# Kernel tuning notes

Measured on AMD Instinct MI355X. Metric: run time of the kernel, lower is better.

## Reference

```python
import jax, jax.numpy as jnp
import numpy as np

N_NODES = 100000
N_EDGES = 3200000
NUM_FEATURES = 512
HIDDEN = 16
NUM_CLASSES = 32


def _gcn_conv(x, src, dst, norm, W, b, n):
    # PyG GCNConv: linear transform first, then normalized scatter-add aggregation
    xw = x @ W                          # [N, out]
    msg = xw[src] * norm[:, None]       # gather over edges (incl. self-loops)
    agg = jax.ops.segment_sum(msg, dst, num_segments=n)
    return agg + b


def setup_inputs() -> dict:
    key = jax.random.key(0)
    k_x, k_e, k_w1, k_w2 = jax.random.split(key, 4)
    x = jax.random.normal(k_x, (N_NODES, NUM_FEATURES), dtype=jnp.float32)
    edge_index = jax.random.randint(k_e, (2, N_EDGES), 0, N_NODES, dtype=jnp.int64)
    # Glorot-style init for the two GCNConv weights; zero bias (PyG default)
    W1 = jax.random.normal(k_w1, (NUM_FEATURES, HIDDEN), dtype=jnp.float32) * (1.0 / np.sqrt(NUM_FEATURES))
    b1 = jnp.zeros((HIDDEN,), dtype=jnp.float32)
    W2 = jax.random.normal(k_w2, (HIDDEN, NUM_CLASSES), dtype=jnp.float32) * (1.0 / np.sqrt(HIDDEN))
    b2 = jnp.zeros((NUM_CLASSES,), dtype=jnp.float32)
    return {"x": x, "edge_index": edge_index, "W1": W1, "b1": b1, "W2": W2, "b2": b2}


def reference(x, edge_index, W1, b1, W2, b2):
    n = x.shape[0]
    # add self-loops (PyG GCNConv default add_self_loops=True)
    loops = jnp.arange(n, dtype=edge_index.dtype)
    src = jnp.concatenate([edge_index[0], loops])
    dst = jnp.concatenate([edge_index[1], loops])
    # symmetric normalization D^{-1/2} (A+I) D^{-1/2}
    deg = jax.ops.segment_sum(jnp.ones_like(dst, dtype=x.dtype), dst, num_segments=n)
    dinv = jnp.where(deg > 0, jax.lax.rsqrt(deg), 0.0)
    norm = dinv[src] * dinv[dst]        # [E + N]

    h = jax.nn.relu(_gcn_conv(x, src, dst, norm, W1, b1, n))
    # F.dropout(p=0.5, training=self.training): eval mode -> identity
    out = _gcn_conv(h, src, dst, norm, W2, b2, n)
    return (out, h)
```

## Files before the change

kernel.cpp:

```cpp
#include <hip/hip_runtime.h>
#include <hip/hip_fp16.h>


#define NN 100000
#define NE 3200000
#define FIN 512
#define HID 16
#define NCLS 32
#define NB 391
#define NBP 512
#define CAP_B 9216

#define OFF_BCNT  0
#define OFF_START (NBP)
#define OFF_CNT   (NBP + NN)
#define OFF_DINV  (NBP + 2*NN)
#define OFF_EP    (NBP + 3*NN)
#define OFF_XWS   (OFF_EP + NB*CAP_B)
#define OFF_HSC   (OFF_XWS + NN*8)

__global__ __launch_bounds__(512) void k_binA(const int* __restrict__ src,
                                              const int* __restrict__ dst,
                                              int* __restrict__ bcnt,
                                              unsigned* __restrict__ ep) {
    __shared__ int hist[NBP];
    __shared__ int gpos[NBP];
    int tid = threadIdx.x;
    hist[tid] = 0;
    __syncthreads();
    int base = blockIdx.x * 4096;
    unsigned rec[8];
    int meta[8];
#pragma unroll
    for (int k = 0; k < 8; ++k) {
        int e = base + tid + k * 512;
        if (e < NE) {
            int s = __builtin_nontemporal_load(src + e);
            int d = __builtin_nontemporal_load(dst + e);
            int b = d >> 8;
            int p = atomicAdd(&hist[b], 1);
            rec[k] = ((unsigned)s << 8) | (unsigned)(d & 255);
            meta[k] = (p << 9) | b;
        } else meta[k] = -1;
    }
    __syncthreads();
    int v = hist[tid];
    if (v > 0) gpos[tid] = atomicAdd(&bcnt[tid], v);
    __syncthreads();
#pragma unroll
    for (int k = 0; k < 8; ++k) {
        if (meta[k] >= 0) {
            int b = meta[k] & 511;
            int p = meta[k] >> 9;
            ep[b * CAP_B + gpos[b] + p] = rec[k];
        }
    }
}

__global__ __launch_bounds__(256) void k_binB(unsigned* __restrict__ ep,
                                              const int* __restrict__ bcnt,
                                              int* __restrict__ startA,
                                              int* __restrict__ cntA,
                                              float* __restrict__ dinv) {
    __shared__ int nh[256];
    __shared__ int ns[256];
    __shared__ int np_[256];
    __shared__ int esL[CAP_B];
    int tid = threadIdx.x;
    int b = blockIdx.x;
    int gbase = b * CAP_B;
    int bc = bcnt[b];
    if (bc > CAP_B) bc = CAP_B;
    nh[tid] = 0;
    __syncthreads();
    for (int t = tid; t < bc; t += 256)
        atomicAdd(&nh[ep[gbase + t] & 255], 1);
    __syncthreads();
    int v = nh[tid];
    ns[tid] = v;
    __syncthreads();
#pragma unroll
    for (int o = 1; o < 256; o <<= 1) {
        int u = (tid >= o) ? ns[tid - o] : 0;
        __syncthreads();
        ns[tid] += u;
        __syncthreads();
    }
    int ex = ns[tid] - v;
    np_[tid] = ex;
    __syncthreads();
    for (int t = tid; t < bc; t += 256) {
        unsigned r = ep[gbase + t];
        int dl = r & 255;
        int p = atomicAdd(&np_[dl], 1);
        esL[p] = (int)(r >> 8);
    }
    __syncthreads();
    for (int t = tid; t < bc; t += 256)
        ep[gbase + t] = (unsigned)esL[t];
    int node = b * 256 + tid;
    if (node < NN) {
        startA[node] = gbase + ex;
        cntA[node]   = v;
        dinv[node]   = rsqrtf((float)(v + 1));
    }
}

__global__ __launch_bounds__(256) void k_xw(const float* __restrict__ x,
                                            const float* __restrict__ W1,
                                            const float* __restrict__ dinv,
                                            __half* __restrict__ xws) {
    __shared__ float w1[FIN * HID];
    for (int t = threadIdx.x; t < FIN * HID; t += 256) {
        int k = t >> 4, j = t & 15;
        int s = (k * 4 + ((j >> 2) ^ ((k >> 2) & 3))) * 4 + (j & 3);
        w1[s] = W1[t];
    }
    __syncthreads();
    int w  = threadIdx.x >> 6;
    int nl = (threadIdx.x >> 2) & 15;
    int c  = threadIdx.x & 3;
    int n0 = blockIdx.x * 128 + w * 32 + nl;
    int n1 = n0 + 16;
    bool v0 = n0 < NN, v1 = n1 < NN;
    const float4* x4 = reinterpret_cast<const float4*>(x);
    const float4* r0 = x4 + (v0 ? (size_t)n0 * (FIN / 4) : 0);
    const float4* r1 = x4 + (v1 ? (size_t)n1 * (FIN / 4) : 0);
    const float4* wv = reinterpret_cast<const float4*>(w1);
    float a0[HID], a1[HID];
#pragma unroll
    for (int j = 0; j < HID; ++j) { a0[j] = 0.f; a1[j] = 0.f; }
#pragma unroll 4
    for (int t = 0; t < 32; ++t) {
        int qk = c + 4 * t;
        float4 xv0 = r0[qk];
        float4 xv1 = r1[qk];
        const float4* wb = wv + qk * 16;
#pragma unroll
        for (int e = 0; e < 4; ++e) {
            float xe0 = (e == 0) ? xv0.x : (e == 1) ? xv0.y : (e == 2) ? xv0.z : xv0.w;
            float xe1 = (e == 0) ? xv1.x : (e == 1) ? xv1.y : (e == 2) ? xv1.z : xv1.w;
#pragma unroll
            for (int j4 = 0; j4 < 4; ++j4) {
                float4 w4 = wb[e * 4 + (j4 ^ c)];
                a0[j4 * 4 + 0] += xe0 * w4.x;
                a0[j4 * 4 + 1] += xe0 * w4.y;
                a0[j4 * 4 + 2] += xe0 * w4.z;
                a0[j4 * 4 + 3] += xe0 * w4.w;
                a1[j4 * 4 + 0] += xe1 * w4.x;
                a1[j4 * 4 + 1] += xe1 * w4.y;
                a1[j4 * 4 + 2] += xe1 * w4.z;
                a1[j4 * 4 + 3] += xe1 * w4.w;
            }
        }
    }
#pragma unroll
    for (int j = 0; j < HID; ++j) {
        a0[j] += __shfl_xor(a0[j], 1);
        a0[j] += __shfl_xor(a0[j], 2);
        a1[j] += __shfl_xor(a1[j], 1);
        a1[j] += __shfl_xor(a1[j], 2);
    }
    if (c == 0) {
        if (v0) {
            float dv = dinv[n0];
            __half2 hv[8];
#pragma unroll
            for (int k = 0; k < 8; ++k)
                hv[k] = __floats2half2_rn(a0[2 * k] * dv, a0[2 * k + 1] * dv);
            float4* o = reinterpret_cast<float4*>(xws + (size_t)n0 * HID);
            o[0] = *reinterpret_cast<float4*>(&hv[0]);
            o[1] = *reinterpret_cast<float4*>(&hv[4]);
        }
        if (v1) {
            float dv = dinv[n1];
            __half2 hv[8];
#pragma unroll
            for (int k = 0; k < 8; ++k)
                hv[k] = __floats2half2_rn(a1[2 * k] * dv, a1[2 * k + 1] * dv);
            float4* o = reinterpret_cast<float4*>(xws + (size_t)n1 * HID);
            o[0] = *reinterpret_cast<float4*>(&hv[0]);
            o[1] = *reinterpret_cast<float4*>(&hv[4]);
        }
    }
}

__global__ __launch_bounds__(256) void k_gather1(const int* __restrict__ startA,
                                                 const int* __restrict__ cntA,
                                                 const int* __restrict__ esrc,
                                                 const __half2* __restrict__ xws2,
                                                 const float* __restrict__ dinv,
                                                 const float* __restrict__ b1,
                                                 float* __restrict__ hout,
                                                 __half2* __restrict__ hsc2) {
    int wave = (blockIdx.x * 256 + threadIdx.x) >> 6;
    if (wave >= NN) return;
    int i = wave;
    int lane = threadIdx.x & 63;
    int j2 = lane & 7;
    int c = lane >> 3;
    int st = startA[i], en = st + cntA[i];
    float sx[8], sy[8];
#pragma unroll
    for (int k = 0; k < 8; ++k) { sx[k] = 0.f; sy[k] = 0.f; }
    for (int e = st + c; e < en; e += 64) {
        int a[8];
#pragma unroll
        for (int k = 0; k < 8; ++k) {
            int ee = e + 8 * k;
            a[k] = __builtin_nontemporal_load(esrc + (ee < en ? ee : e));
        }
#pragma unroll
        for (int k = 0; k < 8; ++k) {
            float2 f = __half22float2(xws2[a[k] * 8 + j2]);
            bool ok = (e + 8 * k) < en;
            sx[k] += ok ? f.x : 0.f;
            sy[k] += ok ? f.y : 0.f;
        }
    }
    float sumx = ((sx[0] + sx[1]) + (sx[2] + sx[3])) + ((sx[4] + sx[5]) + (sx[6] + sx[7]));
    float sumy = ((sy[0] + sy[1]) + (sy[2] + sy[3])) + ((sy[4] + sy[5]) + (sy[6] + sy[7]));
    sumx += __shfl_xor(sumx, 8);  sumy += __shfl_xor(sumy, 8);
    sumx += __shfl_xor(sumx, 16); sumy += __shfl_xor(sumy, 16);
    sumx += __shfl_xor(sumx, 32); sumy += __shfl_xor(sumy, 32);
    if (c == 0) {
        float dv = dinv[i];
        float2 self = __half22float2(xws2[i * 8 + j2]);
        float vx = b1[2 * j2]     + dv * (sumx + self.x);
        float vy = b1[2 * j2 + 1] + dv * (sumy + self.y);
        float hx = vx > 0.f ? vx : 0.f;
        float hy = vy > 0.f ? vy : 0.f;
        *reinterpret_cast<float2*>(hout + i * HID + 2 * j2) = make_float2(hx, hy);
        hsc2[i * 8 + j2] = __floats2half2_rn(hx * dv, hy * dv);
    }
}

__global__ __launch_bounds__(256) void k_gather2h(const int* __restrict__ startA,
                                                  const int* __restrict__ cntA,
                                                  const int* __restrict__ esrc,
                                                  const __half2* __restrict__ hsc2,
                                                  const float* __restrict__ dinv,
                                                  const float* __restrict__ W2,
                                                  const float* __restrict__ b2,
                                                  float* __restrict__ out) {
    __shared__ float w2s[HID * NCLS];
    __shared__ float b2s[NCLS];
    for (int t = threadIdx.x; t < HID * NCLS; t += 256) w2s[t] = W2[t];
    if (threadIdx.x < NCLS) b2s[threadIdx.x] = b2[threadIdx.x];
    __syncthreads();
    int wave = (blockIdx.x * 256 + threadIdx.x) >> 6;
    if (wave >= NN) return;
    int i = wave;
    int lane = threadIdx.x & 63;
    int j2 = lane & 7;
    int c = lane >> 3;
    int st = startA[i], en = st + cntA[i];
    float sx[8], sy[8];
#pragma unroll
    for (int k = 0; k < 8; ++k) { sx[k] = 0.f; sy[k] = 0.f; }
    for (int e = st + c; e < en; e += 64) {
        int a[8];
#pragma unroll
        for (int k = 0; k < 8; ++k) {
            int ee = e + 8 * k;
            a[k] = __builtin_nontemporal_load(esrc + (ee < en ? ee : e));
        }
#pragma unroll
        for (int k = 0; k < 8; ++k) {
            float2 f = __half22float2(hsc2[a[k] * 8 + j2]);
            bool ok = (e + 8 * k) < en;
            sx[k] += ok ? f.x : 0.f;
            sy[k] += ok ? f.y : 0.f;
        }
    }
    float sumx = ((sx[0] + sx[1]) + (sx[2] + sx[3])) + ((sx[4] + sx[5]) + (sx[6] + sx[7]));
    float sumy = ((sy[0] + sy[1]) + (sy[2] + sy[3])) + ((sy[4] + sy[5]) + (sy[6] + sy[7]));
    sumx += __shfl_xor(sumx, 8);  sumy += __shfl_xor(sumy, 8);
    sumx += __shfl_xor(sumx, 16); sumy += __shfl_xor(sumy, 16);
    sumx += __shfl_xor(sumx, 32); sumy += __shfl_xor(sumy, 32);
    {
        float2 self = __half22float2(hsc2[i * 8 + j2]);
        sumx += self.x;
        sumy += self.y;
    }
    int jo = lane & 31;
    float acc = 0.f;
#pragma unroll
    for (int p = 0; p < 8; ++p) {
        acc += __shfl(sumx, p) * w2s[(2 * p) * NCLS + jo];
        acc += __shfl(sumy, p) * w2s[(2 * p + 1) * NCLS + jo];
    }
    if (lane < 32)
        out[i * NCLS + jo] = b2s[jo] + dinv[i] * acc;
}

extern "C" void kernel_launch(void* const* d_in, const int* in_sizes, int n_in,
                              void* d_out, int out_size, void* d_ws, size_t ws_size,
                              hipStream_t stream) {
    const float* x  = (const float*)d_in[0];
    const int* ei   = (const int*)d_in[1];
    const float* W1 = (const float*)d_in[2];
    const float* b1 = (const float*)d_in[3];
    const float* W2 = (const float*)d_in[4];
    const float* b2 = (const float*)d_in[5];

    const int* src = ei;
    const int* dst = ei + NE;

    int* wsi = (int*)d_ws;
    int*      bcnt  = wsi + OFF_BCNT;
    int*      startA= wsi + OFF_START;
    int*      cntA  = wsi + OFF_CNT;
    float*    dinv  = (float*)(wsi + OFF_DINV);
    unsigned* ep    = (unsigned*)(wsi + OFF_EP);
    __half*   xws   = (__half*)(wsi + OFF_XWS);
    __half2*  xws2  = (__half2*)(wsi + OFF_XWS);
    __half2*  hsc2  = (__half2*)(wsi + OFF_HSC);

    float* outp = (float*)d_out;
    float* hout = outp + NN * NCLS;

    const int B = 256;

    hipMemsetAsync(bcnt, 0, NBP * sizeof(int), stream);
    hipLaunchKernelGGL(k_binA,  dim3((NE + 4095) / 4096), dim3(512), 0, stream, src, dst, bcnt, ep);
    hipLaunchKernelGGL(k_binB,  dim3(NB), dim3(B), 0, stream, ep, bcnt, startA, cntA, dinv);
    hipLaunchKernelGGL(k_xw,    dim3((NN + 127) / 128), dim3(B), 0, stream, x, W1, dinv, xws);
    hipLaunchKernelGGL(k_gather1, dim3((NN * 64 + B - 1) / B), dim3(B), 0, stream,
                       startA, cntA, (const int*)ep, xws2, dinv, b1, hout, hsc2);
    hipLaunchKernelGGL(k_gather2h, dim3((NN * 64 + B - 1) / B), dim3(B), 0, stream,
                       startA, cntA, (const int*)ep, hsc2, dinv, W2, b2, outp);
}
```

Baseline: 202.7 us.

## Stage binned edges in LDS before global scatter; store W1 as half in LDS

The binning kernel now does a block-local prefix sum over bucket counts and sorts records into shared memory by bucket. It then writes them to global memory in bucket-contiguous order, so the scattered global stores become more coalesced. Separately, the x@W1 kernel keeps W1 in shared memory as packed fp16 with an XOR swizzle, which halves LDS footprint and load traffic per FMA. The cost is extra conversion work, a 9-step scan with barriers, and reduced precision on the weights.

```diff
diff --git a/kernel.cpp b/kernel.cpp
--- a/kernel.cpp
+++ b/kernel.cpp
@@ -24,36 +24,57 @@
                                               int* __restrict__ bcnt,
                                               unsigned* __restrict__ ep) {
     __shared__ int hist[NBP];
+    __shared__ int lstart[NBP];
     __shared__ int gpos[NBP];
+    __shared__ unsigned recs[4096];
+    __shared__ unsigned short bkt[4096];
     int tid = threadIdx.x;
     hist[tid] = 0;
     __syncthreads();
     int base = blockIdx.x * 4096;
     unsigned rec[8];
-    int meta[8];
+    int bk[8], pl[8];
 #pragma unroll
     for (int k = 0; k < 8; ++k) {
         int e = base + tid + k * 512;
         if (e < NE) {
             int s = __builtin_nontemporal_load(src + e);
             int d = __builtin_nontemporal_load(dst + e);
-            int b = d >> 8;
-            int p = atomicAdd(&hist[b], 1);
+            bk[k] = d >> 8;
+            pl[k] = atomicAdd(&hist[bk[k]], 1);
             rec[k] = ((unsigned)s << 8) | (unsigned)(d & 255);
-            meta[k] = (p << 9) | b;
-        } else meta[k] = -1;
+        } else bk[k] = -1;
     }
     __syncthreads();
     int v = hist[tid];
+    lstart[tid] = v;
+    __syncthreads();
+#pragma unroll
+    for (int o = 1; o < 512; o <<= 1) {
+        int u = (tid >= o) ? lstart[tid - o] : 0;
+        __syncthreads();
+        lstart[tid] += u;
+        __syncthreads();
+    }
+    int ex = lstart[tid] - v;
     if (v > 0) gpos[tid] = atomicAdd(&bcnt[tid], v);
     __syncthreads();
+    lstart[tid] = ex;
+    __syncthreads();
 #pragma unroll
     for (int k = 0; k < 8; ++k) {
-        if (meta[k] >= 0) {
-            int b = meta[k] & 511;
-            int p = meta[k] >> 9;
-            ep[b * CAP_B + gpos[b] + p] = rec[k];
-        }
+        if (bk[k] >= 0) {
+            int slot = lstart[bk[k]] + pl[k];
+            recs[slot] = rec[k];
+            bkt[slot] = (unsigned short)bk[k];
+        }
+    }
+    __syncthreads();
+    int total = lstart[NBP - 1] + hist[NBP - 1];
+#pragma unroll 2
+    for (int t = tid; t < total; t += 512) {
+        int b = bkt[t];
+        ep[b * CAP_B + gpos[b] + (t - lstart[b])] = recs[t];
     }
 }
 
@@ -110,11 +131,13 @@
                                             const float* __restrict__ W1,
                                             const float* __restrict__ dinv,
                                             __half* __restrict__ xws) {
-    __shared__ float w1[FIN * HID];
+    __shared__ float4 w1h[1024];
     for (int t = threadIdx.x; t < FIN * HID; t += 256) {
         int k = t >> 4, j = t & 15;
-        int s = (k * 4 + ((j >> 2) ^ ((k >> 2) & 3))) * 4 + (j & 3);
-        w1[s] = W1[t];
+        int u = (k >> 1) * 4 + (j >> 2);
+        int us = u ^ ((u >> 3) & 7);
+        char* p = (char*)w1h + us * 16 + (j & 3) * 4 + (k & 1) * 2;
+        *(__half*)p = __float2half(W1[t]);
     }
     __syncthreads();
     int w  = threadIdx.x >> 6;
@@ -126,7 +149,6 @@
     const float4* x4 = reinterpret_cast<const float4*>(x);
     const float4* r0 = x4 + (v0 ? (size_t)n0 * (FIN / 4) : 0);
     const float4* r1 = x4 + (v1 ? (size_t)n1 * (FIN / 4) : 0);
-    const float4* wv = reinterpret_cast<const float4*>(w1);
     float a0[HID], a1[HID];
 #pragma unroll
     for (int j = 0; j < HID; ++j) { a0[j] = 0.f; a1[j] = 0.f; }
@@ -135,22 +157,27 @@
         int qk = c + 4 * t;
         float4 xv0 = r0[qk];
         float4 xv1 = r1[qk];
-        const float4* wb = wv + qk * 16;
-#pragma unroll
-        for (int e = 0; e < 4; ++e) {
-            float xe0 = (e == 0) ? xv0.x : (e == 1) ? xv0.y : (e == 2) ? xv0.z : xv0.w;
-            float xe1 = (e == 0) ? xv1.x : (e == 1) ? xv1.y : (e == 2) ? xv1.z : xv1.w;
-#pragma unroll
-            for (int j4 = 0; j4 < 4; ++j4) {
-                float4 w4 = wb[e * 4 + (j4 ^ c)];
-                a0[j4 * 4 + 0] += xe0 * w4.x;
-                a0[j4 * 4 + 1] += xe0 * w4.y;
-                a0[j4 * 4 + 2] += xe0 * w4.z;
-                a0[j4 * 4 + 3] += xe0 * w4.w;
-                a1[j4 * 4 + 0] += xe1 * w4.x;
-                a1[j4 * 4 + 1] += xe1 * w4.y;
-                a1[j4 * 4 + 2] += xe1 * w4.z;
-                a1[j4 * 4 + 3] += xe1 * w4.w;
+#pragma unroll
+        for (int d = 0; d < 2; ++d) {
+            int kp = 2 * qk + d;
+            float ex0 = d ? xv0.z : xv0.x, ey0 = d ? xv0.w : xv0.y;
+            float ex1 = d ? xv1.z : xv1.x, ey1 = d ? xv1.w : xv1.y;
+#pragma unroll
+            for (int jh = 0; jh < 2; ++jh) {
+#pragma unroll
+                for (int q = 0; q < 2; ++q) {
+                    int u = kp * 4 + jh * 2 + q;
+                    int us = u ^ ((u >> 3) & 7);
+                    float4 fv = w1h[us];
+                    const __half2* hp = reinterpret_cast<const __half2*>(&fv);
+#pragma unroll
+                    for (int m = 0; m < 4; ++m) {
+                        float2 f = __half22float2(hp[m]);
+                        int j = jh * 8 + q * 4 + m;
+                        a0[j] += ex0 * f.x + ey0 * f.y;
+                        a1[j] += ex1 * f.x + ey1 * f.y;
+                    }
+                }
             }
         }
     }
```

After: 209.1 us. 3.1% more time.
